# Kernel tuning notes

Measured on AMD Instinct MI355X. Metric: run time of the kernel, lower is better.

Reference implementation:

```python
import jax, jax.numpy as jnp
import numpy as np

E = 64      # embedding_dim
H = 64      # h_dim
MLP = 1024  # mlp_dim (attention hidden)
PRE1 = 512  # mlp_pre_pool hidden
BNK = 1024  # bottleneck_dim
S = 256     # num scenes (equal-size groups replacing seq_start_end)
P = 16      # pedestrians per scene
B = S * P   # total batch of pedestrians
T = 8       # obs_len for vx/vy (only last row used)
EPS = 1e-5  # BatchNorm eps


def _bn(x, g, b, m, v):
    # eval-mode BatchNorm1d over the last (feature) axis
    return (x - m) * jax.lax.rsqrt(v + EPS) * g + b


def setup_inputs() -> dict:
    key = jax.random.key(0)
    ks = jax.random.split(key, 24)
    def n(k, shape, s=1.0):
        return jax.random.normal(k, shape, jnp.float32) * s
    return {
        "h_states": n(ks[0], (1, B, H)),
        "end_pos": n(ks[1], (B, 2)),
        "vx": n(ks[2], (T, B)),
        "vy": n(ks[3], (T, B)),
        "W_sp": n(ks[4], (2, E), 0.05), "b_sp": jnp.zeros((E,), jnp.float32),
        "W_vel": n(ks[5], (2, E), 0.05), "b_vel": jnp.zeros((E,), jnp.float32),
        "Wa1": n(ks[6], (2 * E, MLP), 0.05), "ba1": jnp.zeros((MLP,), jnp.float32),
        "ga1": jnp.ones((MLP,), jnp.float32), "bta1": jnp.zeros((MLP,), jnp.float32),
        "ma1": n(ks[7], (MLP,), 0.1), "va1": jax.random.uniform(ks[8], (MLP,), jnp.float32) + 0.5,
        "Wa2": n(ks[9], (MLP, 1), 0.05), "ba2": jnp.zeros((1,), jnp.float32),
        "ga2": jnp.ones((1,), jnp.float32), "bta2": jnp.zeros((1,), jnp.float32),
        "ma2": n(ks[10], (1,), 0.1), "va2": jax.random.uniform(ks[11], (1,), jnp.float32) + 0.5,
        "Wp1": n(ks[12], (E + H, PRE1), 0.05), "bp1": jnp.zeros((PRE1,), jnp.float32),
        "gp1": jnp.ones((PRE1,), jnp.float32), "btp1": jnp.zeros((PRE1,), jnp.float32),
        "mp1": n(ks[13], (PRE1,), 0.1), "vp1": jax.random.uniform(ks[14], (PRE1,), jnp.float32) + 0.5,
        "Wp2": n(ks[15], (PRE1, BNK), 0.05), "bp2": jnp.zeros((BNK,), jnp.float32),
        "gp2": jnp.ones((BNK,), jnp.float32), "btp2": jnp.zeros((BNK,), jnp.float32),
        "mp2": n(ks[16], (BNK,), 0.1), "vp2": jax.random.uniform(ks[17], (BNK,), jnp.float32) + 0.5,
        "num_scenes": S, "num_ped": P,
    }


def _forward(h_states, end_pos, vx, vy, W_sp, b_sp, W_vel, b_vel,
             Wa1, ba1, ga1, bta1, ma1, va1, Wa2, ba2, ga2, bta2, ma2, va2,
             Wp1, bp1, gp1, btp1, mp1, vp1, Wp2, bp2, gp2, btp2, mp2, vp2,
             num_scenes, num_ped):
    Sn, Pn = num_scenes, num_ped
    h = h_states.reshape(-1, H).reshape(Sn, Pn, H)          # per-scene hidden
    pos = end_pos.reshape(Sn, Pn, 2)
    # rel[s,i,j] = pos[s,j] - pos[s,i]  (repeat vs repeat_interleave in torch)
    rel = pos[:, None, :, :] - pos[:, :, None, :]
    rel_emb = rel @ W_sp + b_sp                              # [S,P,P,E]
    vel = jnp.stack([vx[-1], vy[-1]], axis=-1).reshape(Sn, Pn, 2)
    vel_emb = vel @ W_vel + b_vel                            # [S,P,E], indexed by row i
    vel_emb = jnp.broadcast_to(vel_emb[:, :, None, :], (Sn, Pn, Pn, E))
    att_in = jnp.concatenate([rel_emb, vel_emb], axis=-1)    # [S,P,P,2E]
    a = jax.nn.relu(_bn(att_in @ Wa1 + ba1, ga1, bta1, ma1, va1))
    scores = jax.nn.relu(_bn(a @ Wa2 + ba2, ga2, bta2, ma2, va2))  # [S,P,P,1]
    # torch.softmax(scores, dim=1) on an (N,1) tensor: softmax over the size-1
    # feature axis -> identically 1.0. Reproduced faithfully here.
    w = jax.nn.softmax(scores, axis=-1)
    h_rep = jnp.broadcast_to(h[:, None, :, :], (Sn, Pn, Pn, H))   # h[s,j] per (i,j)
    x = jnp.concatenate([rel_emb, h_rep], axis=-1) * (0.05 * w)   # [S,P,P,E+H]
    y = jax.nn.relu(_bn(x @ Wp1 + bp1, gp1, btp1, mp1, vp1))
    y = jax.nn.relu(_bn(y @ Wp2 + bp2, gp2, btp2, mp2, vp2))      # [S,P,P,BNK]
    pool = jnp.max(y, axis=2)                                     # max over neighbors j
    return pool.reshape(Sn * Pn, BNK)


def reference(h_states, end_pos, vx, vy, W_sp, b_sp, W_vel, b_vel,
              Wa1, ba1, ga1, bta1, ma1, va1, Wa2, ba2, ga2, bta2, ma2, va2,
              Wp1, bp1, gp1, btp1, mp1, vp1, Wp2, bp2, gp2, btp2, mp2, vp2,
              num_scenes, num_ped):
    return _forward(h_states, end_pos, vx, vy, W_sp, b_sp, W_vel, b_vel,
                    Wa1, ba1, ga1, bta1, ma1, va1, Wa2, ba2, ga2, bta2, ma2, va2,
                    Wp1, bp1, gp1, btp1, mp1, vp1, Wp2, bp2, gp2, btp2, mp2, vp2,
                    num_scenes, num_ped)
```

## Files before the change

### kernel.cpp

```cpp
#include <hip/hip_runtime.h>
#include <hip/hip_bf16.h>
#include <stdint.h>
#include <utility>


typedef __bf16 bf16x8 __attribute__((ext_vector_type(8)));
typedef __bf16 bf16x2 __attribute__((ext_vector_type(2)));
typedef float  f32x4  __attribute__((ext_vector_type(4)));
typedef float  f32x2  __attribute__((ext_vector_type(2)));
typedef float  f32x16 __attribute__((ext_vector_type(16)));

#define BP2_OFF 0u
#define BP1_OFF 1048576u
#define MX_OFF  1114112u
#define MY_OFF  1116160u
#define CB_OFF  1118208u
#define SH_OFF  1120256u
#define A2_OFF  1122304u
#define C2_OFF  1126400u

#define Y1_LDS  0
#define HH_LDS  131072
#define LDS_SZ  147456

#define WAITCNT(S) do { asm volatile("s_waitcnt " S ::: "memory"); \
                        __builtin_amdgcn_sched_barrier(0); } while (0)

__device__ __forceinline__ unsigned short f2bf(float f) {
    union { float f; unsigned u; } c; c.f = f;
    unsigned u = c.u;
    return (unsigned short)((u + 0x7fffu + ((u >> 16) & 1u)) >> 16);
}
__device__ __forceinline__ float bfbits2f(unsigned hi) {
    union { unsigned u; float f; } c; c.u = hi; return c.f;
}
__device__ __forceinline__ unsigned pk_bf16(float a, float b) {
#if __has_builtin(__builtin_amdgcn_cvt_pk_bf16_f32)
    bf16x2 p = __builtin_amdgcn_cvt_pk_bf16_f32(a, b);
    union { bf16x2 v; unsigned u; } c; c.v = p; return c.u;
#else
    return (unsigned)f2bf(a) | ((unsigned)f2bf(b) << 16);
#endif
}
__device__ __forceinline__ int y1off(int r, int c16) {
    return r * 1024 + ((c16 ^ (r & 7)) << 4);
}

template<class F, int... Is>
__device__ __forceinline__ void sf_impl(F& f, std::integer_sequence<int, Is...>) {
    (f(std::integral_constant<int, Is>{}), ...);
}
template<int N, class F>
__device__ __forceinline__ void static_for(F&& f) {
    sf_impl(f, std::make_integer_sequence<int, N>{});
}

__global__ __launch_bounds__(256) void prep_pack_kernel(
    const float* __restrict__ Wsp,  const float* __restrict__ bsp,
    const float* __restrict__ Wp1,  const float* __restrict__ bp1,
    const float* __restrict__ gp1,  const float* __restrict__ btp1,
    const float* __restrict__ mp1,  const float* __restrict__ vp1,
    const float* __restrict__ Wp2,  const float* __restrict__ bp2,
    const float* __restrict__ gp2,  const float* __restrict__ btp2,
    const float* __restrict__ mp2,  const float* __restrict__ vp2,
    unsigned char* __restrict__ ws)
{
    __shared__ float tile[32 * 65];
    __shared__ float part[3][4][64];
    const int blk = blockIdx.x, t = threadIdx.x;

    if (blk < 272) {
        const float* src; int ncols, kb, ng;
        if (blk < 256) { kb = blk >> 4; ng = blk & 15; src = Wp2; ncols = 1024; }
        else { int b2 = blk - 256; kb = b2 >> 3; ng = b2 & 7; src = Wp1 + 64 * 512; ncols = 512; }
        const int k0 = kb * 32, n0 = ng * 64;
        #pragma unroll
        for (int it = 0; it < 2; ++it) {
            int c = t + it * 256;
            int r = c >> 4, c4 = c & 15;
            float4 v = *(const float4*)(src + (k0 + r) * ncols + n0 + c4 * 4);
            tile[r * 65 + c4 * 4 + 0] = v.x;
            tile[r * 65 + c4 * 4 + 1] = v.y;
            tile[r * 65 + c4 * 4 + 2] = v.z;
            tile[r * 65 + c4 * 4 + 3] = v.w;
        }
        __syncthreads();
        if (blk < 256) {
            const int l = t & 63, ch = (t >> 6) & 1, kh = t >> 7;
            const int nl = ch * 32 + (l & 31);
            const int kl = kh * 16 + ((l >> 5) & 1) * 8;
            uint4 o;
            o.x = pk_bf16(tile[(kl + 0) * 65 + nl], tile[(kl + 1) * 65 + nl]);
            o.y = pk_bf16(tile[(kl + 2) * 65 + nl], tile[(kl + 3) * 65 + nl]);
            o.z = pk_bf16(tile[(kl + 4) * 65 + nl], tile[(kl + 5) * 65 + nl]);
            o.w = pk_bf16(tile[(kl + 6) * 65 + nl], tile[(kl + 7) * 65 + nl]);
            const int kstep = kb * 2 + kh, ct = ng * 2 + ch;
            ((uint4*)(ws + BP2_OFF))[(kstep * 32 + ct) * 64 + l] = o;
        } else {
            int ntl = t >> 6, l = t & 63;
            int nl = ntl * 16 + (l & 15), kl = (l >> 4) * 8;
            uint4 o;
            o.x = pk_bf16(tile[(kl + 0) * 65 + nl], tile[(kl + 1) * 65 + nl]);
            o.y = pk_bf16(tile[(kl + 2) * 65 + nl], tile[(kl + 3) * 65 + nl]);
            o.z = pk_bf16(tile[(kl + 4) * 65 + nl], tile[(kl + 5) * 65 + nl]);
            o.w = pk_bf16(tile[(kl + 6) * 65 + nl], tile[(kl + 7) * 65 + nl]);
            ((uint4*)(ws + BP1_OFF))[((ng * 4 + ntl) * 2 + kb) * 64 + l] = o;
        }
    } else if (blk < 280) {
        const int kk = t & 63, eq = t >> 6;
        const int k = (blk - 272) * 64 + kk;
        float mx = 0.f, my = 0.f, cb = 0.f;
        #pragma unroll
        for (int e2 = 0; e2 < 16; ++e2) {
            int e = eq * 16 + e2;
            float wv = Wp1[e * 512 + k];
            mx = fmaf(Wsp[e],      wv, mx);
            my = fmaf(Wsp[64 + e], wv, my);
            cb = fmaf(bsp[e],      wv, cb);
        }
        part[0][eq][kk] = mx; part[1][eq][kk] = my; part[2][eq][kk] = cb;
        __syncthreads();
        if (t < 64) {
            const int k2 = (blk - 272) * 64 + t;
            float mxs = part[0][0][t] + part[0][1][t] + part[0][2][t] + part[0][3][t];
            float mys = part[1][0][t] + part[1][1][t] + part[1][2][t] + part[1][3][t];
            float cbs = part[2][0][t] + part[2][1][t] + part[2][2][t] + part[2][3][t];
            float a1 = gp1[k2] * rsqrtf(vp1[k2] + 1e-5f);
            ((float*)(ws + MX_OFF))[k2] = 0.05f * a1 * mxs;
            ((float*)(ws + MY_OFF))[k2] = 0.05f * a1 * mys;
            ((float*)(ws + CB_OFF))[k2] = 0.05f * a1 * cbs + (bp1[k2] - mp1[k2]) * a1 + btp1[k2];
            ((float*)(ws + SH_OFF))[k2] = 0.05f * a1;
        }
    } else {
        int n = (blk - 280) * 256 + t;
        float a = gp2[n] * rsqrtf(vp2[n] + 1e-5f);
        ((float*)(ws + A2_OFF))[n] = a;
        ((float*)(ws + C2_OFF))[n] = btp2[n] + (bp2[n] - mp2[n]) * a;
    }
}

__global__ __launch_bounds__(1024, 4) void mm4_kernel(
    const float* __restrict__ hst,
    const float* __restrict__ epos,
    const unsigned char* __restrict__ ws,
    float* __restrict__ out)
{
    __shared__ __align__(16) unsigned char smem[LDS_SZ];

    const int s   = blockIdx.x >> 1;
    const int ih  = blockIdx.x & 1;
    const int tid = threadIdx.x;
    const int w    = tid >> 6;
    const int l    = tid & 63;
    const int quad = l >> 4;
    const int jl   = l & 15;

    {
        union { unsigned u[4]; bf16x8 v; } afh[2];
        #pragma unroll
        for (int kb = 0; kb < 2; ++kb) {
            const float4* hp = (const float4*)(hst + (s * 16 + jl) * 64 + kb * 32 + quad * 8);
            float4 v0 = hp[0], v1 = hp[1];
            afh[kb].u[0] = pk_bf16(v0.x, v0.y);
            afh[kb].u[1] = pk_bf16(v0.z, v0.w);
            afh[kb].u[2] = pk_bf16(v1.x, v1.y);
            afh[kb].u[3] = pk_bf16(v1.z, v1.w);
        }
        const f32x4 fz = {0.f, 0.f, 0.f, 0.f};
        f32x4 acch[2] = {fz, fz};
        #pragma unroll
        for (int kb = 0; kb < 2; ++kb) {
            #pragma unroll
            for (int ct = 0; ct < 2; ++ct) {
                bf16x8 bfr = *(const bf16x8*)(ws + BP1_OFF + ((((w * 2 + ct) * 2 + kb) * 64 + l) << 4));
                acch[ct] = __builtin_amdgcn_mfma_f32_16x16x32_bf16(afh[kb].v, bfr, acch[ct], 0, 0, 0);
            }
        }
        const float* SHg = (const float*)(ws + SH_OFF);
        const float* CBg = (const float*)(ws + CB_OFF);
        #pragma unroll
        for (int ct = 0; ct < 2; ++ct) {
            int col = (w * 2 + ct) * 16 + jl;
            float sh = SHg[col], cb = CBg[col];
            #pragma unroll
            for (int reg = 0; reg < 4; ++reg) {
                int j = quad * 4 + reg;
                float hv = fmaf(acch[ct][reg], sh, cb);
                *(unsigned short*)(smem + HH_LDS + j * 1024 + col * 2) = f2bf(hv);
            }
        }
    }
    __syncthreads();

    {
        const int i4 = tid >> 8;
        const int j  = (tid >> 4) & 15;
        const int kc = tid & 15;
        float rx[2], ry[2];
        float pjx = epos[s * 32 + j * 2], pjy = epos[s * 32 + j * 2 + 1];
        #pragma unroll
        for (int ii = 0; ii < 2; ++ii) {
            int ig_ = ih * 8 + i4 * 2 + ii;
            rx[ii] = pjx - epos[s * 32 + ig_ * 2];
            ry[ii] = pjy - epos[s * 32 + ig_ * 2 + 1];
        }
        const f32x2 zero2 = {0.f, 0.f};
        #pragma unroll
        for (int kk = 0; kk < 4; ++kk) {
            int c16 = kk * 16 + kc;
            int k = c16 * 8;
            uint4 hh8 = *(const uint4*)(smem + HH_LDS + j * 1024 + k * 2);
            f32x4 mx0 = *(const f32x4*)(ws + MX_OFF + k * 4);
            f32x4 mx1 = *(const f32x4*)(ws + MX_OFF + k * 4 + 16);
            f32x4 my0 = *(const f32x4*)(ws + MY_OFF + k * 4);
            f32x4 my1 = *(const f32x4*)(ws + MY_OFF + k * 4 + 16);
            f32x2 mxp[4] = { {mx0[0],mx0[1]}, {mx0[2],mx0[3]}, {mx1[0],mx1[1]}, {mx1[2],mx1[3]} };
            f32x2 myp[4] = { {my0[0],my0[1]}, {my0[2],my0[3]}, {my1[0],my1[1]}, {my1[2],my1[3]} };
            f32x2 hhp[4];
            hhp[0][0] = bfbits2f(hh8.x << 16); hhp[0][1] = bfbits2f(hh8.x & 0xffff0000u);
            hhp[1][0] = bfbits2f(hh8.y << 16); hhp[1][1] = bfbits2f(hh8.y & 0xffff0000u);
            hhp[2][0] = bfbits2f(hh8.z << 16); hhp[2][1] = bfbits2f(hh8.z & 0xffff0000u);
            hhp[3][0] = bfbits2f(hh8.w << 16); hhp[3][1] = bfbits2f(hh8.w & 0xffff0000u);
            #pragma unroll
            for (int ii = 0; ii < 2; ++ii) {
                f32x2 rx2 = { rx[ii], rx[ii] };
                f32x2 ry2 = { ry[ii], ry[ii] };
                uint4 o;
                unsigned uu[4];
                #pragma unroll
                for (int p = 0; p < 4; ++p) {
                    f32x2 tt = __builtin_elementwise_fma(ry2, myp[p], hhp[p]);
                    tt = __builtin_elementwise_fma(rx2, mxp[p], tt);
                    tt = __builtin_elementwise_max(tt, zero2);
                    uu[p] = pk_bf16(tt[0], tt[1]);
                }
                o.x = uu[0]; o.y = uu[1]; o.z = uu[2]; o.w = uu[3];
                int r = (i4 * 2 + ii) * 16 + j;
                *(uint4*)(smem + Y1_LDS + y1off(r, c16)) = o;
            }
        }
    }
    __syncthreads();

    {
        const int lane31 = l & 31;
        const int hi = l >> 5;
        const int sr = lane31 & 7;
        const int rg = w >> 3;
        const int cg = w & 7;
        const float* A2 = (const float*)(ws + A2_OFF);
        const float* C2 = (const float*)(ws + C2_OFF);

        int av[2];
        #pragma unroll
        for (int rr = 0; rr < 2; ++rr)
            av[rr] = Y1_LDS + ((rg * 2 + rr) * 32 + lane31) * 1024 + ((hi ^ sr) << 4);

        const unsigned char* bp = ws + BP2_OFF + ((cg * 2) << 10) + (l << 4);

        const f32x16 fz16 = {0.f,0.f,0.f,0.f,0.f,0.f,0.f,0.f,
                             0.f,0.f,0.f,0.f,0.f,0.f,0.f,0.f};
        f32x16 acc[2][2];
        bf16x8 ar[2][2];
        bf16x8 br[2][2];

        #pragma unroll
        for (int rr = 0; rr < 2; ++rr) { acc[rr][0] = fz16; acc[rr][1] = fz16; }

        auto epilogue = [&](int pass) {
            #pragma unroll
            for (int c = 0; c < 2; ++c) {
                const int col = (pass * 16 + cg * 2 + c) * 32 + lane31;
                const float a2 = A2[col], c2 = C2[col];
                #pragma unroll
                for (int rr = 0; rr < 2; ++rr) {
                    float mv[2];
                    #pragma unroll
                    for (int hg = 0; hg < 2; ++hg) {
                        float v0 = fmaxf(fmaf(acc[rr][c][hg * 8 + 0], a2, c2), 0.f);
                        float v1 = fmaxf(fmaf(acc[rr][c][hg * 8 + 1], a2, c2), 0.f);
                        float v2 = fmaxf(fmaf(acc[rr][c][hg * 8 + 2], a2, c2), 0.f);
                        float v3 = fmaxf(fmaf(acc[rr][c][hg * 8 + 3], a2, c2), 0.f);
                        float v4 = fmaxf(fmaf(acc[rr][c][hg * 8 + 4], a2, c2), 0.f);
                        float v5 = fmaxf(fmaf(acc[rr][c][hg * 8 + 5], a2, c2), 0.f);
                        float v6 = fmaxf(fmaf(acc[rr][c][hg * 8 + 6], a2, c2), 0.f);
                        float v7 = fmaxf(fmaf(acc[rr][c][hg * 8 + 7], a2, c2), 0.f);
                        float m = fmaxf(fmaxf(fmaxf(v0, v1), fmaxf(v2, v3)),
                                        fmaxf(fmaxf(v4, v5), fmaxf(v6, v7)));
                        mv[hg] = fmaxf(m, __shfl_xor(m, 32, 64));
                    }
                    const int iloc = (rg * 2 + rr) * 2 + hi;
                    const float vout = hi ? mv[1] : mv[0];
                    const int orow = s * 16 + ih * 8 + iloc;
                    __builtin_nontemporal_store(vout, &out[orow * 1024 + col]);
                }
            }
        };

        auto issueG = [&](auto Gc) {
            constexpr int GN = decltype(Gc)::value;
            constexpr int pn = GN >> 5, kn = GN & 31, sl = GN & 1;
            const unsigned char* b = bp + (pn * 16384 + kn * 32768);
            br[sl][0] = *(const bf16x8*)(b);
            br[sl][1] = *(const bf16x8*)(b + 1024);
            constexpr int add = (kn >> 2) * 128;
            constexpr int xr  = (kn & 3) << 5;
            #pragma unroll
            for (int rr = 0; rr < 2; ++rr)
                ar[sl][rr] = *(const bf16x8*)(smem + ((av[rr] + add) ^ xr));
        };

        auto stepG = [&](auto Gc) {
            constexpr int G = decltype(Gc)::value;
            if constexpr (G + 1 <= 63)
                issueG(std::integral_constant<int, G + 1>{});
            if constexpr (G == 32)
                asm volatile("s_waitcnt vmcnt(10) lgkmcnt(2)" ::: "memory");
            else if constexpr (G == 63)
                asm volatile("s_waitcnt vmcnt(0) lgkmcnt(0)" ::: "memory");
            else
                asm volatile("s_waitcnt vmcnt(2) lgkmcnt(2)" ::: "memory");
            __builtin_amdgcn_sched_barrier(0);
            constexpr int sl = G & 1;
            #pragma unroll
            for (int c = 0; c < 2; ++c)
                #pragma unroll
                for (int rr = 0; rr < 2; ++rr)
                    acc[rr][c] = __builtin_amdgcn_mfma_f32_32x32x16_bf16(
                        ar[sl][rr], br[sl][c], acc[rr][c], 0, 0, 0);
        };

        issueG(std::integral_constant<int, 0>{});

        static_for<32>(stepG);
        __builtin_amdgcn_sched_barrier(0);
        epilogue(0);
        #pragma unroll
        for (int rr = 0; rr < 2; ++rr) { acc[rr][0] = fz16; acc[rr][1] = fz16; }
        __builtin_amdgcn_sched_barrier(0);
        static_for<32>([&](auto kc) {
            stepG(std::integral_constant<int, decltype(kc)::value + 32>{});
        });
        __builtin_amdgcn_sched_barrier(0);
        epilogue(1);
    }
}

extern "C" void kernel_launch(void* const* d_in, const int* in_sizes, int n_in,
                              void* d_out, int out_size, void* d_ws, size_t ws_size,
                              hipStream_t stream) {
    const float* hst  = (const float*)d_in[0];
    const float* epos = (const float*)d_in[1];
    const float* Wsp  = (const float*)d_in[4];
    const float* bsp  = (const float*)d_in[5];
    const float* Wp1  = (const float*)d_in[20];
    const float* bp1  = (const float*)d_in[21];
    const float* gp1  = (const float*)d_in[22];
    const float* btp1 = (const float*)d_in[23];
    const float* mp1  = (const float*)d_in[24];
    const float* vp1  = (const float*)d_in[25];
    const float* Wp2  = (const float*)d_in[26];
    const float* bp2  = (const float*)d_in[27];
    const float* gp2  = (const float*)d_in[28];
    const float* btp2 = (const float*)d_in[29];
    const float* mp2  = (const float*)d_in[30];
    const float* vp2  = (const float*)d_in[31];
    unsigned char* ws = (unsigned char*)d_ws;
    float* out = (float*)d_out;

    prep_pack_kernel<<<284, 256, 0, stream>>>(Wsp, bsp, Wp1, bp1, gp1, btp1, mp1, vp1,
                                              Wp2, bp2, gp2, btp2, mp2, vp2, ws);
    mm4_kernel<<<512, 1024, 0, stream>>>(hst, epos, ws, out);
}
```

Baseline: 191.9 us.

## Shrink block to 4 waves with 4x4 MFMA tiles per wave

Reduces the main kernel from 16 waves to 4 waves per block. Each wave now computes a 4x4 grid of 32x32 MFMA tiles instead of 2x2, and the first-layer and elementwise stages are redistributed to match. The larger register tile raises reuse of each loaded A and B fragment and cuts redundant global weight loads per block. In exchange it uses far more accumulator registers and gives lower occupancy, with fewer waves available to hide latency.

```diff
diff --git a/kernel.cpp b/kernel.cpp
--- a/kernel.cpp
+++ b/kernel.cpp
@@ -22,9 +22,6 @@
 #define Y1_LDS  0
 #define HH_LDS  131072
 #define LDS_SZ  147456
-
-#define WAITCNT(S) do { asm volatile("s_waitcnt " S ::: "memory"); \
-                        __builtin_amdgcn_sched_barrier(0); } while (0)
 
 __device__ __forceinline__ unsigned short f2bf(float f) {
     union { float f; unsigned u; } c; c.f = f;
@@ -139,7 +136,7 @@
     }
 }
 
-__global__ __launch_bounds__(1024, 4) void mm4_kernel(
+__global__ __launch_bounds__(256, 1) void mm5_kernel(
     const float* __restrict__ hst,
     const float* __restrict__ epos,
     const unsigned char* __restrict__ ws,
@@ -167,20 +164,20 @@
             afh[kb].u[3] = pk_bf16(v1.z, v1.w);
         }
         const f32x4 fz = {0.f, 0.f, 0.f, 0.f};
-        f32x4 acch[2] = {fz, fz};
+        f32x4 acch[8] = {fz, fz, fz, fz, fz, fz, fz, fz};
         #pragma unroll
         for (int kb = 0; kb < 2; ++kb) {
             #pragma unroll
-            for (int ct = 0; ct < 2; ++ct) {
-                bf16x8 bfr = *(const bf16x8*)(ws + BP1_OFF + ((((w * 2 + ct) * 2 + kb) * 64 + l) << 4));
+            for (int ct = 0; ct < 8; ++ct) {
+                bf16x8 bfr = *(const bf16x8*)(ws + BP1_OFF + ((((w * 8 + ct) * 2 + kb) * 64 + l) << 4));
                 acch[ct] = __builtin_amdgcn_mfma_f32_16x16x32_bf16(afh[kb].v, bfr, acch[ct], 0, 0, 0);
             }
         }
         const float* SHg = (const float*)(ws + SH_OFF);
         const float* CBg = (const float*)(ws + CB_OFF);
         #pragma unroll
-        for (int ct = 0; ct < 2; ++ct) {
-            int col = (w * 2 + ct) * 16 + jl;
+        for (int ct = 0; ct < 8; ++ct) {
+            int col = (w * 8 + ct) * 16 + jl;
             float sh = SHg[col], cb = CBg[col];
             #pragma unroll
             for (int reg = 0; reg < 4; ++reg) {
@@ -193,14 +190,13 @@
     __syncthreads();
 
     {
-        const int i4 = tid >> 8;
-        const int j  = (tid >> 4) & 15;
+        const int j  = tid >> 4;
         const int kc = tid & 15;
-        float rx[2], ry[2];
+        float rx[8], ry[8];
         float pjx = epos[s * 32 + j * 2], pjy = epos[s * 32 + j * 2 + 1];
         #pragma unroll
-        for (int ii = 0; ii < 2; ++ii) {
-            int ig_ = ih * 8 + i4 * 2 + ii;
+        for (int ii = 0; ii < 8; ++ii) {
+            int ig_ = ih * 8 + ii;
             rx[ii] = pjx - epos[s * 32 + ig_ * 2];
             ry[ii] = pjy - epos[s * 32 + ig_ * 2 + 1];
         }
@@ -222,7 +218,7 @@
             hhp[2][0] = bfbits2f(hh8.z << 16); hhp[2][1] = bfbits2f(hh8.z & 0xffff0000u);
             hhp[3][0] = bfbits2f(hh8.w << 16); hhp[3][1] = bfbits2f(hh8.w & 0xffff0000u);
             #pragma unroll
-            for (int ii = 0; ii < 2; ++ii) {
+            for (int ii = 0; ii < 8; ++ii) {
                 f32x2 rx2 = { rx[ii], rx[ii] };
                 f32x2 ry2 = { ry[ii], ry[ii] };
                 uint4 o;
@@ -235,7 +231,7 @@
                     uu[p] = pk_bf16(tt[0], tt[1]);
                 }
                 o.x = uu[0]; o.y = uu[1]; o.z = uu[2]; o.w = uu[3];
-                int r = (i4 * 2 + ii) * 16 + j;
+                int r = ii * 16 + j;
                 *(uint4*)(smem + Y1_LDS + y1off(r, c16)) = o;
             }
         }
@@ -246,50 +242,50 @@
         const int lane31 = l & 31;
         const int hi = l >> 5;
         const int sr = lane31 & 7;
-        const int rg = w >> 3;
-        const int cg = w & 7;
         const float* A2 = (const float*)(ws + A2_OFF);
         const float* C2 = (const float*)(ws + C2_OFF);
 
-        int av[2];
-        #pragma unroll
-        for (int rr = 0; rr < 2; ++rr)
-            av[rr] = Y1_LDS + ((rg * 2 + rr) * 32 + lane31) * 1024 + ((hi ^ sr) << 4);
-
-        const unsigned char* bp = ws + BP2_OFF + ((cg * 2) << 10) + (l << 4);
+        int av[4];
+        #pragma unroll
+        for (int rt = 0; rt < 4; ++rt)
+            av[rt] = Y1_LDS + (rt * 32 + lane31) * 1024 + ((hi ^ sr) << 4);
+
+        const unsigned char* bp = ws + BP2_OFF + ((w * 4) << 10) + (l << 4);
 
         const f32x16 fz16 = {0.f,0.f,0.f,0.f,0.f,0.f,0.f,0.f,
                              0.f,0.f,0.f,0.f,0.f,0.f,0.f,0.f};
-        f32x16 acc[2][2];
-        bf16x8 ar[2][2];
-        bf16x8 br[2][2];
-
-        #pragma unroll
-        for (int rr = 0; rr < 2; ++rr) { acc[rr][0] = fz16; acc[rr][1] = fz16; }
+        f32x16 acc[4][4];
+        bf16x8 ar[2][4];
+        bf16x8 br[2][4];
+
+        #pragma unroll
+        for (int rt = 0; rt < 4; ++rt)
+            #pragma unroll
+            for (int c = 0; c < 4; ++c) acc[rt][c] = fz16;
 
         auto epilogue = [&](int pass) {
             #pragma unroll
-            for (int c = 0; c < 2; ++c) {
-                const int col = (pass * 16 + cg * 2 + c) * 32 + lane31;
+            for (int c = 0; c < 4; ++c) {
+                const int col = (pass * 16 + w * 4 + c) * 32 + lane31;
                 const float a2 = A2[col], c2 = C2[col];
                 #pragma unroll
-                for (int rr = 0; rr < 2; ++rr) {
+                for (int rt = 0; rt < 4; ++rt) {
                     float mv[2];
                     #pragma unroll
                     for (int hg = 0; hg < 2; ++hg) {
-                        float v0 = fmaxf(fmaf(acc[rr][c][hg * 8 + 0], a2, c2), 0.f);
-                        float v1 = fmaxf(fmaf(acc[rr][c][hg * 8 + 1], a2, c2), 0.f);
-                        float v2 = fmaxf(fmaf(acc[rr][c][hg * 8 + 2], a2, c2), 0.f);
-                        float v3 = fmaxf(fmaf(acc[rr][c][hg * 8 + 3], a2, c2), 0.f);
-                        float v4 = fmaxf(fmaf(acc[rr][c][hg * 8 + 4], a2, c2), 0.f);
-                        float v5 = fmaxf(fmaf(acc[rr][c][hg * 8 + 5], a2, c2), 0.f);
-                        float v6 = fmaxf(fmaf(acc[rr][c][hg * 8 + 6], a2, c2), 0.f);
-                        float v7 = fmaxf(fmaf(acc[rr][c][hg * 8 + 7], a2, c2), 0.f);
+                        float v0 = fmaxf(fmaf(acc[rt][c][hg * 8 + 0], a2, c2), 0.f);
+                        float v1 = fmaxf(fmaf(acc[rt][c][hg * 8 + 1], a2, c2), 0.f);
+                        float v2 = fmaxf(fmaf(acc[rt][c][hg * 8 + 2], a2, c2), 0.f);
+                        float v3 = fmaxf(fmaf(acc[rt][c][hg * 8 + 3], a2, c2), 0.f);
+                        float v4 = fmaxf(fmaf(acc[rt][c][hg * 8 + 4], a2, c2), 0.f);
+                        float v5 = fmaxf(fmaf(acc[rt][c][hg * 8 + 5], a2, c2), 0.f);
+                        float v6 = fmaxf(fmaf(acc[rt][c][hg * 8 + 6], a2, c2), 0.f);
+                        float v7 = fmaxf(fmaf(acc[rt][c][hg * 8 + 7], a2, c2), 0.f);
                         float m = fmaxf(fmaxf(fmaxf(v0, v1), fmaxf(v2, v3)),
                                         fmaxf(fmaxf(v4, v5), fmaxf(v6, v7)));
                         mv[hg] = fmaxf(m, __shfl_xor(m, 32, 64));
                     }
-                    const int iloc = (rg * 2 + rr) * 2 + hi;
+                    const int iloc = rt * 2 + hi;
                     const float vout = hi ? mv[1] : mv[0];
                     const int orow = s * 16 + ih * 8 + iloc;
                     __builtin_nontemporal_store(vout, &out[orow * 1024 + col]);
@@ -301,13 +297,14 @@
             constexpr int GN = decltype(Gc)::value;
             constexpr int pn = GN >> 5, kn = GN & 31, sl = GN & 1;
             const unsigned char* b = bp + (pn * 16384 + kn * 32768);
-            br[sl][0] = *(const bf16x8*)(b);
-            br[sl][1] = *(const bf16x8*)(b + 1024);
+            #pragma unroll
+            for (int c = 0; c < 4; ++c)
+                br[sl][c] = *(const bf16x8*)(b + c * 1024);
             constexpr int add = (kn >> 2) * 128;
             constexpr int xr  = (kn & 3) << 5;
             #pragma unroll
-            for (int rr = 0; rr < 2; ++rr)
-                ar[sl][rr] = *(const bf16x8*)(smem + ((av[rr] + add) ^ xr));
+            for (int rt = 0; rt < 4; ++rt)
+                ar[sl][rt] = *(const bf16x8*)(smem + ((av[rt] + add) ^ xr));
         };
 
         auto stepG = [&](auto Gc) {
@@ -315,19 +312,19 @@
             if constexpr (G + 1 <= 63)
                 issueG(std::integral_constant<int, G + 1>{});
             if constexpr (G == 32)
-                asm volatile("s_waitcnt vmcnt(10) lgkmcnt(2)" ::: "memory");
+                asm volatile("s_waitcnt vmcnt(28) lgkmcnt(4)" ::: "memory");
             else if constexpr (G == 63)
                 asm volatile("s_waitcnt vmcnt(0) lgkmcnt(0)" ::: "memory");
             else
-                asm volatile("s_waitcnt vmcnt(2) lgkmcnt(2)" ::: "memory");
+                asm volatile("s_waitcnt vmcnt(4) lgkmcnt(4)" ::: "memory");
             __builtin_amdgcn_sched_barrier(0);
             constexpr int sl = G & 1;
             #pragma unroll
-            for (int c = 0; c < 2; ++c)
+            for (int c = 0; c < 4; ++c)
                 #pragma unroll
-                for (int rr = 0; rr < 2; ++rr)
-                    acc[rr][c] = __builtin_amdgcn_mfma_f32_32x32x16_bf16(
-                        ar[sl][rr], br[sl][c], acc[rr][c], 0, 0, 0);
+                for (int rt = 0; rt < 4; ++rt)
+                    acc[rt][c] = __builtin_amdgcn_mfma_f32_32x32x16_bf16(
+                        ar[sl][rt], br[sl][c], acc[rt][c], 0, 0, 0);
         };
 
         issueG(std::integral_constant<int, 0>{});
@@ -336,7 +333,9 @@
         __builtin_amdgcn_sched_barrier(0);
         epilogue(0);
         #pragma unroll
-        for (int rr = 0; rr < 2; ++rr) { acc[rr][0] = fz16; acc[rr][1] = fz16; }
+        for (int rt = 0; rt < 4; ++rt)
+            #pragma unroll
+            for (int c = 0; c < 4; ++c) acc[rt][c] = fz16;
         __builtin_amdgcn_sched_barrier(0);
         static_for<32>([&](auto kc) {
             stepG(std::integral_constant<int, decltype(kc)::value + 32>{});
@@ -370,5 +369,5 @@
 
     prep_pack_kernel<<<284, 256, 0, stream>>>(Wsp, bsp, Wp1, bp1, gp1, btp1, mp1, vp1,
                                               Wp2, bp2, gp2, btp2, mp2, vp2, ws);
-    mm4_kernel<<<512, 1024, 0, stream>>>(hst, epos, ws, out);
-}
+    mm5_kernel<<<512, 256, 0, stream>>>(hst, epos, ws, out);
+}
```

Result: faster. 183.0 us (-4.7%).
